# Kernel tuning notes

Measured on AMD Instinct MI355X. Metric: run time of the kernel, lower is better.

Reference implementation:

```python
import jax, jax.numpy as jnp
import numpy as np

N_ATOMS = 10000
N_DIH = 8000
N_FRAMES = 2048
EPS = 1e-12  # torch F.normalize eps


def _normalize(v, axis):
    n = jnp.sqrt(jnp.sum(v * v, axis=axis, keepdims=True))
    return v / jnp.maximum(n, EPS)


def setup_inputs() -> dict:
    key = jax.random.key(0)
    k1, k2 = jax.random.split(key)
    x = jax.random.normal(k1, (N_ATOMS * 3 * N_FRAMES,), dtype=jnp.float32)
    atoms = jax.random.randint(k2, (N_DIH, 4), 0, N_ATOMS, dtype=jnp.int32)
    return {"input": x, "atoms": atoms}


def reference(input, atoms):
    geoms = input.reshape(N_ATOMS, 3, -1)          # (n_atoms, 3, B)
    g = geoms[atoms]                               # (n_dih, 4, 3, B) gather
    a12 = _normalize(g[:, 1] - g[:, 0], axis=1)    # (n_dih, 3, B)
    a23 = _normalize(g[:, 2] - g[:, 1], axis=1)
    a34 = _normalize(g[:, 3] - g[:, 2], axis=1)
    vp1 = jnp.cross(a12, a23, axis=1)
    vp2 = jnp.cross(a23, a34, axis=1)
    vp3 = jnp.cross(vp1, a23, axis=1)
    sp1 = jnp.sum(vp1 * vp2, axis=1)               # (n_dih, B)
    sp2 = jnp.sum(vp3 * vp2, axis=1)
    st = jnp.stack([-sp2, sp1])                    # (2, n_dih, B)
    out = _normalize(st, axis=0)
    return out.reshape(2 * atoms.shape[0], -1)     # (2*n_dih, B)
```

## Files before the change

kernel.cpp:

```cpp
#include <hip/hip_runtime.h>

#define N_ATOMS 10000
#define N_DIH   8000
#define NB      2048
#define EPS     1e-12f

typedef float f4_t __attribute__((ext_vector_type(4)));

__global__ __launch_bounds__(256) void dihedral_kernel(
    const float* __restrict__ x,
    const int*   __restrict__ atoms,
    float*       __restrict__ out)
{
    const int bid  = blockIdx.x;
    const int d    = (bid < N_DIH) ? bid : (bid - N_DIH);
    const int half = (bid < N_DIH) ? 0 : 1024;
    const int b    = half + (threadIdx.x << 2);

    const int4 aidx = *reinterpret_cast<const int4*>(atoms + d * 4);
    const int ai[4] = {aidx.x, aidx.y, aidx.z, aidx.w};

    float4 g[4][3];
#pragma unroll
    for (int j = 0; j < 4; ++j) {
        const float* base = x + (size_t)ai[j] * (3 * NB) + b;
#pragma unroll
        for (int c = 0; c < 3; ++c) {
            g[j][c] = *reinterpret_cast<const float4*>(base + c * NB);
        }
    }

    f4_t v0, v1;
#pragma unroll
    for (int k = 0; k < 4; ++k) {
        float p[4][3];
#pragma unroll
        for (int j = 0; j < 4; ++j) {
            p[j][0] = reinterpret_cast<const float*>(&g[j][0])[k];
            p[j][1] = reinterpret_cast<const float*>(&g[j][1])[k];
            p[j][2] = reinterpret_cast<const float*>(&g[j][2])[k];
        }

        float a12[3], a23[3], a34[3];
#pragma unroll
        for (int c = 0; c < 3; ++c) {
            a12[c] = p[1][c] - p[0][c];
            a23[c] = p[2][c] - p[1][c];
            a34[c] = p[3][c] - p[2][c];
        }
        {
            float n12 = sqrtf(a12[0]*a12[0] + a12[1]*a12[1] + a12[2]*a12[2]);
            float n23 = sqrtf(a23[0]*a23[0] + a23[1]*a23[1] + a23[2]*a23[2]);
            float n34 = sqrtf(a34[0]*a34[0] + a34[1]*a34[1] + a34[2]*a34[2]);
            float i12 = 1.0f / fmaxf(n12, EPS);
            float i23 = 1.0f / fmaxf(n23, EPS);
            float i34 = 1.0f / fmaxf(n34, EPS);
#pragma unroll
            for (int c = 0; c < 3; ++c) { a12[c] *= i12; a23[c] *= i23; a34[c] *= i34; }
        }

        float vp1[3], vp2[3], vp3[3];
        vp1[0] = a12[1]*a23[2] - a12[2]*a23[1];
        vp1[1] = a12[2]*a23[0] - a12[0]*a23[2];
        vp1[2] = a12[0]*a23[1] - a12[1]*a23[0];

        vp2[0] = a23[1]*a34[2] - a23[2]*a34[1];
        vp2[1] = a23[2]*a34[0] - a23[0]*a34[2];
        vp2[2] = a23[0]*a34[1] - a23[1]*a34[0];

        vp3[0] = vp1[1]*a23[2] - vp1[2]*a23[1];
        vp3[1] = vp1[2]*a23[0] - vp1[0]*a23[2];
        vp3[2] = vp1[0]*a23[1] - vp1[1]*a23[0];

        float sp1 = vp1[0]*vp2[0] + vp1[1]*vp2[1] + vp1[2]*vp2[2];
        float sp2 = vp3[0]*vp2[0] + vp3[1]*vp2[1] + vp3[2]*vp2[2];

        float s2  = sp1*sp1 + sp2*sp2;
        float inv = __builtin_amdgcn_rsqf(fmaxf(s2, 1e-24f));
        v0[k] = -sp2 * inv;
        v1[k] =  sp1 * inv;
    }

    __builtin_nontemporal_store(v0, reinterpret_cast<f4_t*>(out + (size_t)d * NB + b));
    __builtin_nontemporal_store(v1, reinterpret_cast<f4_t*>(out + (size_t)(N_DIH + d) * NB + b));
}

extern "C" void kernel_launch(void* const* d_in, const int* in_sizes, int n_in,
                              void* d_out, int out_size, void* d_ws, size_t ws_size,
                              hipStream_t stream) {
    const float* x     = (const float*)d_in[0];
    const int*   atoms = (const int*)d_in[1];
    float*       out   = (float*)d_out;

    const int grid  = 2 * N_DIH;
    const int block = 256;
    dihedral_kernel<<<grid, block, 0, stream>>>(x, atoms, out);
}
```

Baseline: 134.1 us.

## Assign one wavefront per dihedral with double-buffered register prefetch loop

Restructures the work split so each 64-lane wavefront handles one full dihedral across all 2048 frames in eight chunks, instead of a 256-thread block covering half the frames. Loads for the next chunk are issued into a second register buffer while the current chunk is computed, aiming to hide gather latency. It also drops the nontemporal stores for plain stores and sets launch bounds to 3 blocks per CU. The cost is higher register pressure from two 12-vector buffers and fewer blocks in flight, which could reduce occupancy.

```diff
diff --git a/kernel.cpp b/kernel.cpp
--- a/kernel.cpp
+++ b/kernel.cpp
@@ -7,38 +7,19 @@
 
 typedef float f4_t __attribute__((ext_vector_type(4)));
 
-__global__ __launch_bounds__(256) void dihedral_kernel(
-    const float* __restrict__ x,
-    const int*   __restrict__ atoms,
-    float*       __restrict__ out)
+__device__ __forceinline__ void compute_store_unit(
+    const f4_t* __restrict__ g,
+    int fg, float* __restrict__ o0base, float* __restrict__ o1base)
 {
-    const int bid  = blockIdx.x;
-    const int d    = (bid < N_DIH) ? bid : (bid - N_DIH);
-    const int half = (bid < N_DIH) ? 0 : 1024;
-    const int b    = half + (threadIdx.x << 2);
-
-    const int4 aidx = *reinterpret_cast<const int4*>(atoms + d * 4);
-    const int ai[4] = {aidx.x, aidx.y, aidx.z, aidx.w};
-
-    float4 g[4][3];
-#pragma unroll
-    for (int j = 0; j < 4; ++j) {
-        const float* base = x + (size_t)ai[j] * (3 * NB) + b;
-#pragma unroll
-        for (int c = 0; c < 3; ++c) {
-            g[j][c] = *reinterpret_cast<const float4*>(base + c * NB);
-        }
-    }
-
     f4_t v0, v1;
 #pragma unroll
     for (int k = 0; k < 4; ++k) {
         float p[4][3];
 #pragma unroll
         for (int j = 0; j < 4; ++j) {
-            p[j][0] = reinterpret_cast<const float*>(&g[j][0])[k];
-            p[j][1] = reinterpret_cast<const float*>(&g[j][1])[k];
-            p[j][2] = reinterpret_cast<const float*>(&g[j][2])[k];
+            p[j][0] = g[j * 3 + 0][k];
+            p[j][1] = g[j * 3 + 1][k];
+            p[j][2] = g[j * 3 + 2][k];
         }
 
         float a12[3], a23[3], a34[3];
@@ -81,8 +62,57 @@
         v1[k] =  sp1 * inv;
     }
 
-    __builtin_nontemporal_store(v0, reinterpret_cast<f4_t*>(out + (size_t)d * NB + b));
-    __builtin_nontemporal_store(v1, reinterpret_cast<f4_t*>(out + (size_t)(N_DIH + d) * NB + b));
+    *reinterpret_cast<f4_t*>(o0base + (fg << 2)) = v0;
+    *reinterpret_cast<f4_t*>(o1base + (fg << 2)) = v1;
+}
+
+__global__ __launch_bounds__(256, 3) void dihedral_kernel(
+    const float* __restrict__ x,
+    const int*   __restrict__ atoms,
+    float*       __restrict__ out)
+{
+    const int lane = threadIdx.x & 63;
+    const int d = __builtin_amdgcn_readfirstlane(blockIdx.x * 4 + (threadIdx.x >> 6));
+
+    const int4 aidx = *reinterpret_cast<const int4*>(atoms + (size_t)d * 4);
+    const float* __restrict__ r0 = x + (size_t)aidx.x * (3 * NB);
+    const float* __restrict__ r1 = x + (size_t)aidx.y * (3 * NB);
+    const float* __restrict__ r2 = x + (size_t)aidx.z * (3 * NB);
+    const float* __restrict__ r3 = x + (size_t)aidx.w * (3 * NB);
+
+    float* __restrict__ o0base = out + (size_t)d * NB;
+    float* __restrict__ o1base = out + (size_t)(N_DIH + d) * NB;
+
+    f4_t bufA[12], bufB[12];
+
+#define LOADU(BUF, I) do {                                                   \
+        const int fo_ = (((I) * 64 + lane) << 2);                            \
+        (BUF)[0]  = *reinterpret_cast<const f4_t*>(r0 + 0 * NB + fo_);       \
+        (BUF)[1]  = *reinterpret_cast<const f4_t*>(r0 + 1 * NB + fo_);       \
+        (BUF)[2]  = *reinterpret_cast<const f4_t*>(r0 + 2 * NB + fo_);       \
+        (BUF)[3]  = *reinterpret_cast<const f4_t*>(r1 + 0 * NB + fo_);       \
+        (BUF)[4]  = *reinterpret_cast<const f4_t*>(r1 + 1 * NB + fo_);       \
+        (BUF)[5]  = *reinterpret_cast<const f4_t*>(r1 + 2 * NB + fo_);       \
+        (BUF)[6]  = *reinterpret_cast<const f4_t*>(r2 + 0 * NB + fo_);       \
+        (BUF)[7]  = *reinterpret_cast<const f4_t*>(r2 + 1 * NB + fo_);       \
+        (BUF)[8]  = *reinterpret_cast<const f4_t*>(r2 + 2 * NB + fo_);       \
+        (BUF)[9]  = *reinterpret_cast<const f4_t*>(r3 + 0 * NB + fo_);       \
+        (BUF)[10] = *reinterpret_cast<const f4_t*>(r3 + 1 * NB + fo_);       \
+        (BUF)[11] = *reinterpret_cast<const f4_t*>(r3 + 2 * NB + fo_);       \
+    } while (0)
+
+    LOADU(bufA, 0);
+#pragma unroll
+    for (int i = 0; i < 8; ++i) {
+        if ((i & 1) == 0) {
+            if (i < 7) LOADU(bufB, i + 1);
+            compute_store_unit(bufA, i * 64 + lane, o0base, o1base);
+        } else {
+            if (i < 7) LOADU(bufA, i + 1);
+            compute_store_unit(bufB, i * 64 + lane, o0base, o1base);
+        }
+    }
+#undef LOADU
 }
 
 extern "C" void kernel_launch(void* const* d_in, const int* in_sizes, int n_in,
@@ -92,7 +122,5 @@
     const int*   atoms = (const int*)d_in[1];
     float*       out   = (float*)d_out;
 
-    const int grid  = 2 * N_DIH;
-    const int block = 256;
-    dihedral_kernel<<<grid, block, 0, stream>>>(x, atoms, out);
+    dihedral_kernel<<<2000, 256, 0, stream>>>(x, atoms, out);
 }
```

After: 136.9 us. 1.02x slower.
